# Optimization experiments

Measured on AMD Instinct MI355X. Metric: run time of the kernel, lower is better.

Reference implementation:

```python
import jax, jax.numpy as jnp
import numpy as np

N_NODES = 100000
N_GRAPHS = 512
D_IN = 300
D_HID = 300
D_OUT = 128  # 2 * SEQUENCE_LENGTH


def _gcn_norm(edge_index, n):
    # PyG GCNConv default: add self-loops, symmetric normalization
    src, dst = edge_index[0], edge_index[1]
    loop = jnp.arange(n, dtype=src.dtype)
    src = jnp.concatenate([src, loop])
    dst = jnp.concatenate([dst, loop])
    deg = jax.ops.segment_sum(jnp.ones_like(dst, dtype=jnp.float32), dst, num_segments=n)
    dinv = jnp.where(deg > 0, jax.lax.rsqrt(deg), 0.0)
    norm = dinv[src] * dinv[dst]  # [E+N]
    return src, dst, norm


def _gcn_conv(x, src, dst, norm, W, b, n):
    h = x @ W                              # transform first (PyG order)
    msg = norm[:, None] * h[src]           # gather + scale, [E+N, D]
    agg = jax.ops.segment_sum(msg, dst, num_segments=n)  # scatter-add
    return agg + b


def setup_inputs() -> dict:
    key = jax.random.key(0)
    ks = jax.random.split(key, 10)
    x = jax.random.normal(ks[0], (N_NODES, D_IN), dtype=jnp.float32)
    edge_index = jax.random.randint(ks[1], (2, 800000), 0, N_NODES, dtype=jnp.int64)
    batch = jnp.sort(jax.random.randint(ks[2], (N_NODES,), 0, N_GRAPHS, dtype=jnp.int64))
    s = 1.0 / np.sqrt(D_IN)
    W1 = jax.random.uniform(ks[3], (D_IN, D_HID), jnp.float32, -s, s)
    b1 = jnp.zeros((D_HID,), jnp.float32)
    W2 = jax.random.uniform(ks[4], (D_HID, D_HID), jnp.float32, -s, s)
    b2 = jnp.zeros((D_HID,), jnp.float32)
    W3 = jax.random.uniform(ks[5], (D_HID, D_OUT), jnp.float32, -s, s)
    b3 = jnp.zeros((D_OUT,), jnp.float32)
    Wm = jax.random.uniform(ks[6], (D_OUT, 1), jnp.float32, -s, s)
    bm = jnp.zeros((1,), jnp.float32)
    return {"x": x, "edge_index": edge_index, "batch": batch,
            "W1": W1, "b1": b1, "W2": W2, "b2": b2,
            "W3": W3, "b3": b3, "Wm": Wm, "bm": bm}


def reference(x, edge_index, batch, W1, b1, W2, b2, W3, b3, Wm, bm):
    n = x.shape[0]
    src, dst, norm = _gcn_norm(edge_index, n)
    # dropout is identity in eval mode
    h = jax.nn.relu(_gcn_conv(x, src, dst, norm, W1, b1, n))
    h = jax.nn.relu(_gcn_conv(h, src, dst, norm, W2, b2, n))
    h = jax.nn.relu(_gcn_conv(h, src, dst, norm, W3, b3, n))
    # global mean pool over graphs
    sums = jax.ops.segment_sum(h, batch, num_segments=N_GRAPHS)
    cnt = jax.ops.segment_sum(jnp.ones((n,), jnp.float32), batch, num_segments=N_GRAPHS)
    readout = sums / jnp.maximum(cnt, 1.0)[:, None]   # [G, D_OUT]
    return (readout @ Wm + bm)[:, 0]                  # [G]
```

## Files before the change

### kernel.cpp

```cpp
#include <hip/hip_runtime.h>
#include <hip/hip_bf16.h>

typedef __bf16 bf16;
typedef __bf16 bf16x4 __attribute__((ext_vector_type(4)));
typedef __bf16 bf16x8 __attribute__((ext_vector_type(8)));
typedef float f32x4 __attribute__((ext_vector_type(4)));

constexpr int N_NODES  = 100000;
constexpr int N_EDGES  = 800000;
constexpr int N_GRAPHS = 512;
constexpr int D_IN  = 300;
constexpr int D_HID = 300;
constexpr int D_OUT = 128;
constexpr int KP    = 320;

#define AS1(p) ((const __attribute__((address_space(1))) void*)(p))
#define AS3(p) ((__attribute__((address_space(3))) void*)(p))


__global__ __launch_bounds__(256) void k_init(int* deg, float* gsum, int* cnt) {
  int i = blockIdx.x * 256 + threadIdx.x;
  if (i < N_NODES) deg[i] = 0;
  if (i < N_GRAPHS) { gsum[i] = 0.f; cnt[i] = 0; }
}

__global__ __launch_bounds__(256) void k_deg(const int* __restrict__ ei, int* __restrict__ deg) {
  int e = blockIdx.x * 256 + threadIdx.x;
  if (e < N_EDGES) atomicAdd(&deg[ei[N_EDGES + e]], 1);
}

__global__ __launch_bounds__(256) void k_dinv(const int* __restrict__ deg, float* __restrict__ dinv) {
  int v = blockIdx.x * 256 + threadIdx.x;
  if (v < N_NODES) dinv[v] = rsqrtf((float)(deg[v] + 1));
}

__global__ __launch_bounds__(256) void k_scan1(const int* __restrict__ deg, int* __restrict__ rp,
                                               int* __restrict__ part) {
  __shared__ int sm[256];
  int tid = threadIdx.x;
  int i = blockIdx.x * 256 + tid;
  int v = (i < N_NODES) ? deg[i] : 0;
  sm[tid] = v;
  __syncthreads();
  for (int off = 1; off < 256; off <<= 1) {
    int t = (tid >= off) ? sm[tid - off] : 0;
    __syncthreads();
    sm[tid] += t;
    __syncthreads();
  }
  if (i < N_NODES) rp[i] = sm[tid] - v;
  if (tid == 255) part[blockIdx.x] = sm[255];
}

__global__ __launch_bounds__(512) void k_scan2(int* part, int nb) {
  __shared__ int sm[512];
  int tid = threadIdx.x;
  int v = (tid < nb) ? part[tid] : 0;
  sm[tid] = v;
  __syncthreads();
  for (int off = 1; off < 512; off <<= 1) {
    int t = (tid >= off) ? sm[tid - off] : 0;
    __syncthreads();
    sm[tid] += t;
    __syncthreads();
  }
  if (tid < nb) part[tid] = sm[tid] - v;
}

__global__ __launch_bounds__(256) void k_scan3(int* __restrict__ rp, const int* __restrict__ part,
                                               int* __restrict__ cur) {
  int i = blockIdx.x * 256 + threadIdx.x;
  if (i < N_NODES) {
    int r = rp[i] + part[blockIdx.x];
    rp[i] = r;
    cur[i] = r;
  }
  if (i == 0) rp[N_NODES] = N_EDGES;
}

__global__ __launch_bounds__(256) void k_fill(const int* __restrict__ ei, int* __restrict__ cur,
                                              int* __restrict__ col) {
  int e = blockIdx.x * 256 + threadIdx.x;
  if (e < N_EDGES) {
    int s = ei[e];
    int d = ei[N_EDGES + e];
    int p = atomicAdd(&cur[d], 1);
    col[p] = s;
  }
}


__global__ __launch_bounds__(256) void k_conv_x(const float* __restrict__ x, const float* __restrict__ dinv,
                                                bf16* __restrict__ Xs) {
  int i = blockIdx.x * 256 + threadIdx.x;
  if (i >= N_NODES * (KP / 4)) return;
  int j = i % (KP / 4);
  int v = i / (KP / 4);
  float4 f = make_float4(0.f, 0.f, 0.f, 0.f);
  if (j < D_IN / 4) f = ((const float4*)(x + (size_t)v * D_IN))[j];
  float dv = dinv[v];
  bf16x4 o;
  o[0] = (bf16)(f.x * dv); o[1] = (bf16)(f.y * dv); o[2] = (bf16)(f.z * dv); o[3] = (bf16)(f.w * dv);
  *(bf16x4*)(Xs + (size_t)v * KP + j * 4) = o;
}

__global__ __launch_bounds__(256) void k_conv_w(const float* __restrict__ W, bf16* __restrict__ Wt,
                                                int Kin, int Nin) {
  int i = blockIdx.x * 256 + threadIdx.x;
  if (i >= KP * KP) return;
  int k = i % KP;
  int n = i / KP;
  float f = (k < Kin && n < Nin) ? W[k * Nin + n] : 0.f;
  Wt[i] = (bf16)f;
}


__global__ __launch_bounds__(256) void k_aggb(const bf16* __restrict__ in, const int* __restrict__ rp,
                                              const int* __restrict__ col, const float* __restrict__ dinv,
                                              bf16* __restrict__ out) {
  int w = threadIdx.x >> 6, l = threadIdx.x & 63;
  int v = blockIdx.x * 4 + w;
  if (v >= N_NODES) return;
  if (l >= 40) return;
  const size_t co = (size_t)8 * l;

  float A0[8], A1[8];
  {
    bf16x8 p = *(const bf16x8*)(in + (size_t)v * KP + co);
#pragma unroll
    for (int j = 0; j < 8; ++j) { A0[j] = (float)p[j]; A1[j] = 0.f; }
  }
  int s = rp[v], e = rp[v + 1];
  int i = s;
  for (; i + 4 <= e; i += 4) {
    int u0 = col[i], u1 = col[i + 1], u2 = col[i + 2], u3 = col[i + 3];
    bf16x8 p0 = *(const bf16x8*)(in + (size_t)u0 * KP + co);
    bf16x8 p1 = *(const bf16x8*)(in + (size_t)u1 * KP + co);
    bf16x8 p2 = *(const bf16x8*)(in + (size_t)u2 * KP + co);
    bf16x8 p3 = *(const bf16x8*)(in + (size_t)u3 * KP + co);
#pragma unroll
    for (int j = 0; j < 8; ++j) {
      A0[j] += (float)p0[j] + (float)p2[j];
      A1[j] += (float)p1[j] + (float)p3[j];
    }
  }
  for (; i + 2 <= e; i += 2) {
    int u0 = col[i], u1 = col[i + 1];
    bf16x8 p0 = *(const bf16x8*)(in + (size_t)u0 * KP + co);
    bf16x8 p1 = *(const bf16x8*)(in + (size_t)u1 * KP + co);
#pragma unroll
    for (int j = 0; j < 8; ++j) { A0[j] += (float)p0[j]; A1[j] += (float)p1[j]; }
  }
  if (i < e) {
    int u0 = col[i];
    bf16x8 p0 = *(const bf16x8*)(in + (size_t)u0 * KP + co);
#pragma unroll
    for (int j = 0; j < 8; ++j) A0[j] += (float)p0[j];
  }
  float dv = dinv[v];
  bf16x8 o;
#pragma unroll
  for (int j = 0; j < 8; ++j) o[j] = (bf16)((A0[j] + A1[j]) * dv);
  *(bf16x8*)(out + (size_t)v * KP + co) = o;
}


template <int NP, int WM, int WN, bool LAST>
__global__ __launch_bounds__(256) void k_gemm(const bf16* __restrict__ A, const bf16* __restrict__ Bt,
                                              const float* __restrict__ dinv, const float* __restrict__ bias,
                                              const float* __restrict__ Wm, bf16* __restrict__ H,
                                              float* __restrict__ sArr) {
  constexpr int WROWS = 64 / WM;
  constexpr int MI    = WROWS / 16;
  constexpr int WCOLS = NP / WN;
  constexpr int NC    = WCOLS / 16;
  constexpr int NB    = NP / 64;
  __shared__ __attribute__((aligned(16))) bf16 sA[64 * 32];
  __shared__ __attribute__((aligned(16))) bf16 sB[NP * 32];
  int m0 = blockIdx.x * 64;
  int tid = threadIdx.x;
  int w = tid >> 6, l = tid & 63;
  int wm = w / WN, wn = w % WN;

  int rA = m0 + w * 16 + (l >> 2);
  if (rA > N_NODES - 1) rA = N_NODES - 1;
  const bf16* gA = A + (size_t)rA * KP + (l & 3) * 8;
  bf16* lA = &sA[w * 512];

  f32x4 acc[MI][NC] = {};
  int la = l & 15, q = l >> 4, kk = q * 8;

  for (int k0 = 0; k0 < KP; k0 += 32) {
    __builtin_amdgcn_global_load_lds(AS1(gA + k0), AS3(lA), 16, 0, 0);
#pragma unroll
    for (int i = 0; i < NB; ++i) {
      int rB = i * 64 + w * 16 + (l >> 2);
      const bf16* gB = Bt + (size_t)rB * KP + k0 + (l & 3) * 8;
      __builtin_amdgcn_global_load_lds(AS1(gB), AS3(&sB[i * 2048 + w * 512]), 16, 0, 0);
    }
    __syncthreads();

    bf16x8 af[MI];
#pragma unroll
    for (int mi = 0; mi < MI; ++mi)
      af[mi] = *(const bf16x8*)&sA[(wm * WROWS + mi * 16 + la) * 32 + kk];
#pragma unroll
    for (int nc = 0; nc < NC; ++nc) {
      bf16x8 bfr = *(const bf16x8*)&sB[(wn * WCOLS + nc * 16 + la) * 32 + kk];
#pragma unroll
      for (int mi = 0; mi < MI; ++mi)
        acc[mi][nc] = __builtin_amdgcn_mfma_f32_16x16x32_bf16(af[mi], bfr, acc[mi][nc], 0, 0, 0);
    }
    __syncthreads();
  }

  int rbase = m0 + wm * WROWS + q * 4;
  if (!LAST) {
    float bc[NC];
#pragma unroll
    for (int nc = 0; nc < NC; ++nc) {
      int c = wn * WCOLS + nc * 16 + la;
      bc[nc] = (c < D_HID) ? bias[c] : 0.f;
    }
#pragma unroll
    for (int mi = 0; mi < MI; ++mi) {
#pragma unroll
      for (int r = 0; r < 4; ++r) {
        int row = rbase + mi * 16 + r;
        if (row < N_NODES) {
          float dv = dinv[row];
#pragma unroll
          for (int nc = 0; nc < NC; ++nc) {
            int c = wn * WCOLS + nc * 16 + la;
            H[(size_t)row * KP + c] = (bf16)(fmaxf(acc[mi][nc][r] + bc[nc], 0.f) * dv);
          }
        }
      }
    }
  } else {
    float bc[NC], wc[NC];
#pragma unroll
    for (int nc = 0; nc < NC; ++nc) {
      int c = nc * 16 + la;
      bc[nc] = bias[c];
      wc[nc] = Wm[c];
    }
    float sv[4];
#pragma unroll
    for (int r = 0; r < 4; ++r) {
      sv[r] = 0.f;
#pragma unroll
      for (int nc = 0; nc < NC; ++nc)
        sv[r] += fmaxf(acc[0][nc][r] + bc[nc], 0.f) * wc[nc];
    }
#pragma unroll
    for (int m = 1; m < 16; m <<= 1) {
#pragma unroll
      for (int r = 0; r < 4; ++r) sv[r] += __shfl_xor(sv[r], m);
    }
    if (la == 0) {
#pragma unroll
      for (int r = 0; r < 4; ++r) {
        int row = rbase + r;
        if (row < N_NODES) sArr[row] = sv[r];
      }
    }
  }
}


__global__ __launch_bounds__(256) void k_gsum(const float* __restrict__ sArr, const int* __restrict__ batch,
                                              float* __restrict__ gsum, int* __restrict__ cnt) {
  __shared__ float lsum[N_GRAPHS];
  __shared__ int   lcnt[N_GRAPHS];
  int tid = threadIdx.x;
  lsum[tid] = 0.f; lsum[tid + 256] = 0.f;
  lcnt[tid] = 0;   lcnt[tid + 256] = 0;
  __syncthreads();
  int v = blockIdx.x * 256 + tid;
  if (v < N_NODES) {
    int b = batch[v];
    atomicAdd(&lsum[b], sArr[v]);
    atomicAdd(&lcnt[b], 1);
  }
  __syncthreads();
  for (int g = tid; g < N_GRAPHS; g += 256) {
    int c = lcnt[g];
    if (c) { atomicAdd(&gsum[g], lsum[g]); atomicAdd(&cnt[g], c); }
  }
}

__global__ __launch_bounds__(512) void k_final(const float* __restrict__ gsum, const int* __restrict__ cnt,
                                               const float* __restrict__ bm, float* __restrict__ out) {
  int g = blockIdx.x * 512 + threadIdx.x;
  if (g < N_GRAPHS) out[g] = gsum[g] / fmaxf((float)cnt[g], 1.f) + bm[0];
}


extern "C" void kernel_launch(void* const* d_in, const int* in_sizes, int n_in,
                              void* d_out, int out_size, void* d_ws, size_t ws_size,
                              hipStream_t stream) {
  const float* x    = (const float*)d_in[0];
  const int*   ei   = (const int*)d_in[1];
  const int*   batch= (const int*)d_in[2];
  const float* W1   = (const float*)d_in[3];
  const float* b1   = (const float*)d_in[4];
  const float* W2   = (const float*)d_in[5];
  const float* b2   = (const float*)d_in[6];
  const float* W3   = (const float*)d_in[7];
  const float* b3   = (const float*)d_in[8];
  const float* Wm   = (const float*)d_in[9];
  const float* bm   = (const float*)d_in[10];
  float* out = (float*)d_out;

  char* ws = (char*)d_ws;
  size_t off = 0;
  auto alloc = [&](size_t bytes) {
    void* p = ws + off;
    off = (off + bytes + 255) & ~(size_t)255;
    return p;
  };
  bf16*  Xs   = (bf16*)alloc((size_t)N_NODES * KP * sizeof(bf16));
  bf16*  Ab   = (bf16*)alloc((size_t)N_NODES * KP * sizeof(bf16));
  bf16*  Wt   = (bf16*)alloc((size_t)KP * KP * sizeof(bf16));
  int*   deg  = (int*)alloc((size_t)N_NODES * 4);
  float* dinv = (float*)alloc((size_t)N_NODES * 4);
  int*   rp   = (int*)alloc((size_t)(N_NODES + 1) * 4);
  int*   cur  = (int*)alloc((size_t)N_NODES * 4);
  int*   col  = (int*)alloc((size_t)N_EDGES * 4);
  int*   part = (int*)alloc(1024 * 4);
  float* sArr = (float*)alloc((size_t)N_NODES * 4);
  float* gsum = (float*)alloc((size_t)N_GRAPHS * 4);
  int*   cnt  = (int*)alloc((size_t)N_GRAPHS * 4);
  bf16*  H    = Xs;

  int nbN = (N_NODES + 255) / 256;
  int nbE = (N_EDGES + 255) / 256;
  int nbA = (N_NODES + 3) / 4;
  int nbG = (N_NODES + 63) / 64;
  int nbW = (KP * KP + 255) / 256;

  k_init<<<nbN, 256, 0, stream>>>(deg, gsum, cnt);
  k_deg<<<nbE, 256, 0, stream>>>(ei, deg);
  k_dinv<<<nbN, 256, 0, stream>>>(deg, dinv);
  k_scan1<<<nbN, 256, 0, stream>>>(deg, rp, part);
  k_scan2<<<1, 512, 0, stream>>>(part, nbN);
  k_scan3<<<nbN, 256, 0, stream>>>(rp, part, cur);
  k_fill<<<nbE, 256, 0, stream>>>(ei, cur, col);
  k_conv_x<<<(N_NODES * (KP / 4) + 255) / 256, 256, 0, stream>>>(x, dinv, Xs);

  k_conv_w<<<nbW, 256, 0, stream>>>(W1, Wt, 300, 300);
  k_aggb<<<nbA, 256, 0, stream>>>(Xs, rp, col, dinv, Ab);
  k_gemm<KP, 2, 2, false><<<nbG, 256, 0, stream>>>(Ab, Wt, dinv, b1, nullptr, H, nullptr);
  k_conv_w<<<nbW, 256, 0, stream>>>(W2, Wt, 300, 300);
  k_aggb<<<nbA, 256, 0, stream>>>(H, rp, col, dinv, Ab);
  k_gemm<KP, 2, 2, false><<<nbG, 256, 0, stream>>>(Ab, Wt, dinv, b2, nullptr, H, nullptr);
  k_conv_w<<<nbW, 256, 0, stream>>>(W3, Wt, 300, 128);
  k_aggb<<<nbA, 256, 0, stream>>>(H, rp, col, dinv, Ab);
  k_gemm<128, 4, 1, true><<<nbG, 256, 0, stream>>>(Ab, Wt, dinv, b3, Wm, nullptr, sArr);

  k_gsum<<<nbN, 256, 0, stream>>>(sArr, batch, gsum, cnt);
  k_final<<<1, 512, 0, stream>>>(gsum, cnt, bm, out);
}
```

Baseline: 518.2 us.

## Enlarge GEMM tiles to 128 rows with 64-wide K steps and swizzled LDS; unroll gather by 8

The GEMM now processes 128-row tiles with 512 threads, loads 64-element K slices per stage (5 stages instead of 10) and XOR-swizzles the LDS layout to avoid bank conflicts. This halves barrier count and improves B-tile reuse across more rows. The node buffers are padded to a multiple of 128 rows so the new loads can skip row clamping. Separately, the aggregation gather loop adds an 8-way unrolled path to keep more loads in flight. Costs include higher LDS use per block (about 56KB for the 320-wide case), which may limit occupancy, and reads from the padded rows, which are never written or initialised.

```diff
diff --git a/kernel.cpp b/kernel.cpp
--- a/kernel.cpp
+++ b/kernel.cpp
@@ -13,6 +13,9 @@
 constexpr int D_HID = 300;
 constexpr int D_OUT = 128;
 constexpr int KP    = 320;
+constexpr int MT    = 128;
+constexpr int NTILE = (N_NODES + MT - 1) / MT;
+constexpr int NPAD  = NTILE * MT;
 
 #define AS1(p) ((const __attribute__((address_space(1))) void*)(p))
 #define AS3(p) ((__attribute__((address_space(3))) void*)(p))
@@ -132,12 +135,26 @@
   }
   int s = rp[v], e = rp[v + 1];
   int i = s;
+  for (; i + 8 <= e; i += 8) {
+    bf16x8 p0 = *(const bf16x8*)(in + (size_t)col[i]     * KP + co);
+    bf16x8 p1 = *(const bf16x8*)(in + (size_t)col[i + 1] * KP + co);
+    bf16x8 p2 = *(const bf16x8*)(in + (size_t)col[i + 2] * KP + co);
+    bf16x8 p3 = *(const bf16x8*)(in + (size_t)col[i + 3] * KP + co);
+    bf16x8 p4 = *(const bf16x8*)(in + (size_t)col[i + 4] * KP + co);
+    bf16x8 p5 = *(const bf16x8*)(in + (size_t)col[i + 5] * KP + co);
+    bf16x8 p6 = *(const bf16x8*)(in + (size_t)col[i + 6] * KP + co);
+    bf16x8 p7 = *(const bf16x8*)(in + (size_t)col[i + 7] * KP + co);
+#pragma unroll
+    for (int j = 0; j < 8; ++j) {
+      A0[j] += ((float)p0[j] + (float)p2[j]) + ((float)p4[j] + (float)p6[j]);
+      A1[j] += ((float)p1[j] + (float)p3[j]) + ((float)p5[j] + (float)p7[j]);
+    }
+  }
   for (; i + 4 <= e; i += 4) {
-    int u0 = col[i], u1 = col[i + 1], u2 = col[i + 2], u3 = col[i + 3];
-    bf16x8 p0 = *(const bf16x8*)(in + (size_t)u0 * KP + co);
-    bf16x8 p1 = *(const bf16x8*)(in + (size_t)u1 * KP + co);
-    bf16x8 p2 = *(const bf16x8*)(in + (size_t)u2 * KP + co);
-    bf16x8 p3 = *(const bf16x8*)(in + (size_t)u3 * KP + co);
+    bf16x8 p0 = *(const bf16x8*)(in + (size_t)col[i]     * KP + co);
+    bf16x8 p1 = *(const bf16x8*)(in + (size_t)col[i + 1] * KP + co);
+    bf16x8 p2 = *(const bf16x8*)(in + (size_t)col[i + 2] * KP + co);
+    bf16x8 p3 = *(const bf16x8*)(in + (size_t)col[i + 3] * KP + co);
 #pragma unroll
     for (int j = 0; j < 8; ++j) {
       A0[j] += (float)p0[j] + (float)p2[j];
@@ -145,15 +162,13 @@
     }
   }
   for (; i + 2 <= e; i += 2) {
-    int u0 = col[i], u1 = col[i + 1];
-    bf16x8 p0 = *(const bf16x8*)(in + (size_t)u0 * KP + co);
-    bf16x8 p1 = *(const bf16x8*)(in + (size_t)u1 * KP + co);
+    bf16x8 p0 = *(const bf16x8*)(in + (size_t)col[i]     * KP + co);
+    bf16x8 p1 = *(const bf16x8*)(in + (size_t)col[i + 1] * KP + co);
 #pragma unroll
     for (int j = 0; j < 8; ++j) { A0[j] += (float)p0[j]; A1[j] += (float)p1[j]; }
   }
   if (i < e) {
-    int u0 = col[i];
-    bf16x8 p0 = *(const bf16x8*)(in + (size_t)u0 * KP + co);
+    bf16x8 p0 = *(const bf16x8*)(in + (size_t)col[i] * KP + co);
 #pragma unroll
     for (int j = 0; j < 8; ++j) A0[j] += (float)p0[j];
   }
@@ -166,55 +181,68 @@
 
 
 template <int NP, int WM, int WN, bool LAST>
-__global__ __launch_bounds__(256) void k_gemm(const bf16* __restrict__ A, const bf16* __restrict__ Bt,
-                                              const float* __restrict__ dinv, const float* __restrict__ bias,
-                                              const float* __restrict__ Wm, bf16* __restrict__ H,
-                                              float* __restrict__ sArr) {
-  constexpr int WROWS = 64 / WM;
+__global__ __launch_bounds__(512, 4) void k_gemm(const bf16* __restrict__ A, const bf16* __restrict__ Bt,
+                                                 const float* __restrict__ dinv, const float* __restrict__ bias,
+                                                 const float* __restrict__ Wm, bf16* __restrict__ H,
+                                                 float* __restrict__ sArr) {
+  constexpr int WROWS = MT / WM;
   constexpr int MI    = WROWS / 16;
   constexpr int WCOLS = NP / WN;
   constexpr int NC    = WCOLS / 16;
-  constexpr int NB    = NP / 64;
-  __shared__ __attribute__((aligned(16))) bf16 sA[64 * 32];
-  __shared__ __attribute__((aligned(16))) bf16 sB[NP * 32];
-  int m0 = blockIdx.x * 64;
-  int tid = threadIdx.x;
-  int w = tid >> 6, l = tid & 63;
-  int wm = w / WN, wn = w % WN;
-
-  int rA = m0 + w * 16 + (l >> 2);
-  if (rA > N_NODES - 1) rA = N_NODES - 1;
-  const bf16* gA = A + (size_t)rA * KP + (l & 3) * 8;
-  bf16* lA = &sA[w * 512];
+  constexpr int NB_B  = NP / 64;
+  __shared__ __attribute__((aligned(16))) char sA[MT * 128];
+  __shared__ __attribute__((aligned(16))) char sB[NP * 128];
+
+  const int tid = threadIdx.x;
+  const int w = tid >> 6, l = tid & 63;
+  const int wm = w / WN, wn = w % WN;
+  const int m0 = blockIdx.x * MT;
+
+  const int sr  = tid >> 3;
+  const int ssw = ((tid & 7) << 4) ^ ((sr & 7) << 4);
+  const char* Ab = (const char*)A;
+  const char* Bb = (const char*)Bt;
+
+  const int la = l & 15, q = l >> 4;
+  const int msk = (la & 7) << 4;
 
   f32x4 acc[MI][NC] = {};
-  int la = l & 15, q = l >> 4, kk = q * 8;
-
-  for (int k0 = 0; k0 < KP; k0 += 32) {
-    __builtin_amdgcn_global_load_lds(AS1(gA + k0), AS3(lA), 16, 0, 0);
-#pragma unroll
-    for (int i = 0; i < NB; ++i) {
-      int rB = i * 64 + w * 16 + (l >> 2);
-      const bf16* gB = Bt + (size_t)rB * KP + k0 + (l & 3) * 8;
-      __builtin_amdgcn_global_load_lds(AS1(gB), AS3(&sB[i * 2048 + w * 512]), 16, 0, 0);
-    }
-    __syncthreads();
-
-    bf16x8 af[MI];
-#pragma unroll
-    for (int mi = 0; mi < MI; ++mi)
-      af[mi] = *(const bf16x8*)&sA[(wm * WROWS + mi * 16 + la) * 32 + kk];
-#pragma unroll
-    for (int nc = 0; nc < NC; ++nc) {
-      bf16x8 bfr = *(const bf16x8*)&sB[(wn * WCOLS + nc * 16 + la) * 32 + kk];
-#pragma unroll
-      for (int mi = 0; mi < MI; ++mi)
-        acc[mi][nc] = __builtin_amdgcn_mfma_f32_16x16x32_bf16(af[mi], bfr, acc[mi][nc], 0, 0, 0);
-    }
-    __syncthreads();
-  }
-
-  int rbase = m0 + wm * WROWS + q * 4;
+
+  for (int kh = 0; kh < 5; ++kh) {
+#pragma unroll
+    for (int i = 0; i < 2; ++i) {
+      const char* src = Ab + (size_t)(m0 + i * 64 + sr) * 640 + kh * 128 + ssw;
+      __builtin_amdgcn_global_load_lds(AS1(src), AS3(sA + i * 8192 + w * 1024), 16, 0, 0);
+    }
+#pragma unroll
+    for (int i = 0; i < NB_B; ++i) {
+      const char* src = Bb + (size_t)(i * 64 + sr) * 640 + kh * 128 + ssw;
+      __builtin_amdgcn_global_load_lds(AS1(src), AS3(sB + i * 8192 + w * 1024), 16, 0, 0);
+    }
+    __syncthreads();
+
+#pragma unroll
+    for (int ks = 0; ks < 2; ++ks) {
+      const int cb = (ks * 64 + q * 16) ^ msk;
+      bf16x8 af[MI];
+#pragma unroll
+      for (int mi = 0; mi < MI; ++mi) {
+        int r = wm * WROWS + mi * 16 + la;
+        af[mi] = *(const bf16x8*)(sA + r * 128 + cb);
+      }
+#pragma unroll
+      for (int nc = 0; nc < NC; ++nc) {
+        int rb = wn * WCOLS + nc * 16 + la;
+        bf16x8 bfr = *(const bf16x8*)(sB + rb * 128 + cb);
+#pragma unroll
+        for (int mi = 0; mi < MI; ++mi)
+          acc[mi][nc] = __builtin_amdgcn_mfma_f32_16x16x32_bf16(af[mi], bfr, acc[mi][nc], 0, 0, 0);
+      }
+    }
+    __syncthreads();
+  }
+
+  const int rbase = m0 + wm * WROWS + q * 4;
   if (!LAST) {
     float bc[NC];
 #pragma unroll
@@ -320,8 +348,8 @@
     off = (off + bytes + 255) & ~(size_t)255;
     return p;
   };
-  bf16*  Xs   = (bf16*)alloc((size_t)N_NODES * KP * sizeof(bf16));
-  bf16*  Ab   = (bf16*)alloc((size_t)N_NODES * KP * sizeof(bf16));
+  bf16*  Xs   = (bf16*)alloc((size_t)NPAD * KP * sizeof(bf16));
+  bf16*  Ab   = (bf16*)alloc((size_t)NPAD * KP * sizeof(bf16));
   bf16*  Wt   = (bf16*)alloc((size_t)KP * KP * sizeof(bf16));
   int*   deg  = (int*)alloc((size_t)N_NODES * 4);
   float* dinv = (float*)alloc((size_t)N_NODES * 4);
@@ -337,7 +365,6 @@
   int nbN = (N_NODES + 255) / 256;
   int nbE = (N_EDGES + 255) / 256;
   int nbA = (N_NODES + 3) / 4;
-  int nbG = (N_NODES + 63) / 64;
   int nbW = (KP * KP + 255) / 256;
 
   k_init<<<nbN, 256, 0, stream>>>(deg, gsum, cnt);
@@ -351,13 +378,13 @@
 
   k_conv_w<<<nbW, 256, 0, stream>>>(W1, Wt, 300, 300);
   k_aggb<<<nbA, 256, 0, stream>>>(Xs, rp, col, dinv, Ab);
-  k_gemm<KP, 2, 2, false><<<nbG, 256, 0, stream>>>(Ab, Wt, dinv, b1, nullptr, H, nullptr);
+  k_gemm<KP, 2, 4, false><<<NTILE, 512, 0, stream>>>(Ab, Wt, dinv, b1, nullptr, H, nullptr);
   k_conv_w<<<nbW, 256, 0, stream>>>(W2, Wt, 300, 300);
   k_aggb<<<nbA, 256, 0, stream>>>(H, rp, col, dinv, Ab);
-  k_gemm<KP, 2, 2, false><<<nbG, 256, 0, stream>>>(Ab, Wt, dinv, b2, nullptr, H, nullptr);
+  k_gemm<KP, 2, 4, false><<<NTILE, 512, 0, stream>>>(Ab, Wt, dinv, b2, nullptr, H, nullptr);
   k_conv_w<<<nbW, 256, 0, stream>>>(W3, Wt, 300, 128);
   k_aggb<<<nbA, 256, 0, stream>>>(H, rp, col, dinv, Ab);
-  k_gemm<128, 4, 1, true><<<nbG, 256, 0, stream>>>(Ab, Wt, dinv, b3, Wm, nullptr, sArr);
+  k_gemm<128, 8, 1, true><<<NTILE, 512, 0, stream>>>(Ab, Wt, dinv, b3, Wm, nullptr, sArr);
 
   k_gsum<<<nbN, 256, 0, stream>>>(sArr, batch, gsum, cnt);
   k_final<<<1, 512, 0, stream>>>(gsum, cnt, bm, out);
```

New measurement: 499.1 us. 1.04x faster.
